# Performance work log

Measured on AMD Instinct MI355X. Metric: run time of the kernel, lower is better.

The kernel has to match this reference:

```python
import jax, jax.numpy as jnp
import numpy as np

MARGIN = 0.5
BETA = 0.0
K = 5

def setup_inputs() -> dict:
    key = jax.random.key(0)
    k1, k2 = jax.random.split(key)
    n, d, n_classes = 4096, 512, 512
    inputs = jax.random.normal(k1, (n, d), dtype=jnp.float32)
    # L2-normalize as is standard for similarity-based DML embeddings
    inputs = inputs / jnp.linalg.norm(inputs, axis=1, keepdims=True)
    targets = jax.random.randint(k2, (n,), 0, n_classes, dtype=jnp.int64)
    return {"inputs": inputs, "targets": targets}

def reference(inputs, targets):
    n = inputs.shape[0]
    sim = inputs @ inputs.T                      # [n, n] similarity matrix
    same = targets[:, None] == targets[None, :]  # [n, n] same-class mask
    eye = jnp.eye(n, dtype=bool)
    pos_mask = same & ~eye                       # positive pairs (off-diagonal)
    neg_mask = ~same                             # negative pairs
    # margin_loss (hinge on similarity): pos -> [margin + beta - s]_+, neg -> [margin + s - beta]_+
    pos_l = jnp.maximum(MARGIN + BETA - sim, 0.0)
    neg_l = jnp.maximum(MARGIN + sim - BETA, 0.0)
    valid = pos_mask | neg_mask
    pair_loss = jnp.where(pos_mask, pos_l, neg_l)  # per-pair loss where valid
    num_of_zeros = jnp.sum(valid & (pair_loss == 0.0))
    # top-(4K) over the multiset of all valid pair losses (== topk of concat(pos_loss, neg_loss))
    masked = jnp.where(valid, pair_loss, -jnp.inf).reshape(-1)
    top_loss, _ = jax.lax.top_k(masked, 4 * K)
    loss = jnp.mean(top_loss)
    mean_pos_sim = jnp.sum(jnp.where(pos_mask, sim, 0.0)) / jnp.sum(pos_mask)
    mean_neg_sim = jnp.sum(jnp.where(neg_mask, sim, 0.0)) / jnp.sum(neg_mask)
    # NOTE: the original swaps the names: it returns mean(pos_sim) as `mean_neg_sim` and vice versa.
    return (loss, num_of_zeros, mean_pos_sim, mean_neg_sim)
```

## Files before the change

### kernel.cpp

```cpp
#include <hip/hip_runtime.h>
#include <hip/hip_fp16.h>

constexpr int N = 4096;
constexpr int D = 512;
constexpr int NT = 64;
constexpr int NBLK = NT * (NT + 1) / 2;
constexpr int NSEG = 32;
constexpr int SEGSZ = NBLK / NSEG;
constexpr float SENT = -1e30f;

typedef _Float16 f16x8 __attribute__((ext_vector_type(8)));
typedef float f32x4 __attribute__((ext_vector_type(4)));

__device__ __forceinline__ void load_lds16(const _Float16* g, _Float16* l) {
  __builtin_amdgcn_global_load_lds(
      (const __attribute__((address_space(1))) void*)g,
      (__attribute__((address_space(3))) void*)l, 16, 0, 0);
}

template <int M>
__device__ __forceinline__ void wave_sel10(float (&vals)[M], float (&out)[10]) {
  int lane = threadIdx.x & 63;
  float lm = vals[0];
#pragma unroll
  for (int k = 1; k < M; k++) lm = fmaxf(lm, vals[k]);
#pragma unroll
  for (int r = 0; r < 10; r++) {
    float wmx = lm;
#pragma unroll
    for (int ofs = 1; ofs < 64; ofs <<= 1)
      wmx = fmaxf(wmx, __shfl_xor(wmx, ofs));
    out[r] = wmx;
    unsigned long long b = __ballot(lm == wmx);
    int leader = __ffsll(b) - 1;
    if (lane == leader) {
      bool found = false;
#pragma unroll
      for (int k = 0; k < M; k++) {
        bool hit = !found && (vals[k] == wmx);
        vals[k] = hit ? SENT : vals[k];
        found = found || hit;
      }
      lm = vals[0];
#pragma unroll
      for (int k = 1; k < M; k++) lm = fmaxf(lm, vals[k]);
    }
  }
}

constexpr int TOP10G_OFF = 41600;
constexpr int STATSL2_OFF = 124800;
constexpr int T10L2_OFF = 125440;
constexpr int DONE2_OFF = 126720;
constexpr int XH_OFF = 126976;

__global__ void prep_kernel(const float4* __restrict__ X4,
                            ushort4* __restrict__ Xh4,
                            unsigned* __restrict__ done2) {
  int gid = blockIdx.x * 256 + threadIdx.x;
  if (gid == 0) *done2 = 0u;
  float4 v = X4[gid];
  ushort4 o;
  o.x = __half_as_ushort(__float2half_rn(v.x));
  o.y = __half_as_ushort(__float2half_rn(v.y));
  o.z = __half_as_ushort(__float2half_rn(v.z));
  o.w = __half_as_ushort(__float2half_rn(v.w));
  Xh4[gid] = o;
}

__global__ __launch_bounds__(256, 4) void gemm_stats_kernel(
    const _Float16* __restrict__ Xh, const int* __restrict__ tgt,
    float* __restrict__ slots, float* __restrict__ top10g) {
  float* blk_sumv = slots;
  float* blk_sump = slots + NBLK;
  unsigned* blk_cntv = (unsigned*)(slots + 2 * NBLK);
  unsigned* blk_cntp = (unsigned*)(slots + 3 * NBLK);
  unsigned* blk_zero = (unsigned*)(slots + 4 * NBLK);

  __shared__ _Float16 As[64 * 64];
  __shared__ _Float16 Bs[64 * 64];
  __shared__ int tA[64], tB[64];
  __shared__ float redf[2][4];
  __shared__ unsigned redu[3][4];
  __shared__ float wml[40];

  int tid = threadIdx.x;

  int id = blockIdx.x, br = 0;
  while (id >= (NT - br)) { id -= (NT - br); br++; }
  int bc = br + id;

  if (tid < 64) tA[tid] = tgt[br * 64 + tid];
  else if (tid < 128) tB[tid - 64] = tgt[bc * 64 + (tid - 64)];

  int lane = tid & 63, wave = tid >> 6;
  int wm = (wave >> 1) << 5;
  int wn = (wave & 1) << 5;
  int lrow = lane & 15;
  int q4 = lane >> 4;
  int x7 = lrow & 7;
  int quad4 = q4 * 4;

  int srow[2], scol[2], sdst[2];
#pragma unroll
  for (int i = 0; i < 2; i++) {
    int C = (i * 4 + wave) * 64 + lane;
    int row = C >> 3, p = C & 7;
    srow[i] = row;
    scol[i] = (p ^ (row & 7)) * 8;
    sdst[i] = (i * 4 + wave) * 512;
  }
  const _Float16* Arow = Xh + (size_t)(br * 64) * D;
  const _Float16* Brow = Xh + (size_t)(bc * 64) * D;

  f32x4 acc[2][2] = {};

  for (int k0 = 0; k0 < D; k0 += 64) {
    __syncthreads();
#pragma unroll
    for (int i = 0; i < 2; i++) {
      load_lds16(Arow + srow[i] * D + k0 + scol[i], As + sdst[i]);
      load_lds16(Brow + srow[i] * D + k0 + scol[i], Bs + sdst[i]);
    }
    __syncthreads();
#pragma unroll
    for (int ks = 0; ks < 64; ks += 32) {
      int c0 = ks >> 3;
      f16x8 af[2], bf[2];
#pragma unroll
      for (int mi = 0; mi < 2; mi++)
        af[mi] = *(const f16x8*)&As[(wm + mi * 16 + lrow) * 64 +
                                    ((c0 + q4) ^ x7) * 8];
#pragma unroll
      for (int ni = 0; ni < 2; ni++)
        bf[ni] = *(const f16x8*)&Bs[(wn + ni * 16 + lrow) * 64 +
                                    ((c0 + q4) ^ x7) * 8];
#pragma unroll
      for (int mi = 0; mi < 2; mi++)
#pragma unroll
        for (int ni = 0; ni < 2; ni++)
          acc[mi][ni] = __builtin_amdgcn_mfma_f32_16x16x32_f16(
              af[mi], bf[ni], acc[mi][ni], 0, 0, 0);
    }
  }

  int ti2[2][4], tj2[2];
#pragma unroll
  for (int ni = 0; ni < 2; ni++) tj2[ni] = tB[wn + ni * 16 + lrow];
#pragma unroll
  for (int mi = 0; mi < 2; mi++)
#pragma unroll
    for (int r = 0; r < 4; r++) ti2[mi][r] = tA[wm + mi * 16 + quad4 + r];

  float lsv = 0.f, lsp = 0.f;
  unsigned lcv = 0, lcp = 0, lz = 0;
  int ibase = br * 64 + wm + quad4;
  int jbase = bc * 64 + wn + lrow;

  float vals[16];
#pragma unroll
  for (int mi = 0; mi < 2; mi++)
#pragma unroll
    for (int ni = 0; ni < 2; ni++)
#pragma unroll
      for (int r = 0; r < 4; r++) {
        float s = acc[mi][ni][r];
        int i = ibase + mi * 16 + r;
        int j = jbase + ni * 16;
        bool valid = j > i;
        bool pos = valid && (ti2[mi][r] == tj2[ni]);
        float t = pos ? -s : s;
        float loss = fmaxf(0.5f + t, 0.0f);
        if (valid) { lsv += s; lcv++; if (loss == 0.0f) lz++; }
        if (pos) { lsp += s; lcp++; }
        vals[(mi * 2 + ni) * 4 + r] = valid ? loss : SENT;
      }

#pragma unroll
  for (int o = 32; o > 0; o >>= 1) {
    lsv += __shfl_down(lsv, o);
    lsp += __shfl_down(lsp, o);
    lcv += __shfl_down(lcv, o);
    lcp += __shfl_down(lcp, o);
    lz  += __shfl_down(lz, o);
  }
  if (lane == 0) {
    redf[0][wave] = lsv; redf[1][wave] = lsp;
    redu[0][wave] = lcv; redu[1][wave] = lcp; redu[2][wave] = lz;
  }

  float wl[10];
  wave_sel10<16>(vals, wl);
  if (lane == 0) {
#pragma unroll
    for (int r = 0; r < 10; r++) wml[wave * 10 + r] = wl[r];
  }
  __syncthreads();

  if (wave == 0) {
    float mv[1];
    mv[0] = (lane < 40) ? wml[lane] : SENT;
    float b10[10];
    wave_sel10<1>(mv, b10);
    if (lane == 0) {
      int b = blockIdx.x;
      blk_sumv[b] = redf[0][0] + redf[0][1] + redf[0][2] + redf[0][3];
      blk_sump[b] = redf[1][0] + redf[1][1] + redf[1][2] + redf[1][3];
      blk_cntv[b] = redu[0][0] + redu[0][1] + redu[0][2] + redu[0][3];
      blk_cntp[b] = redu[1][0] + redu[1][1] + redu[1][2] + redu[1][3];
      blk_zero[b] = redu[2][0] + redu[2][1] + redu[2][2] + redu[2][3];
#pragma unroll
      for (int r = 0; r < 10; r++) top10g[b * 10 + r] = b10[r];
    }
  }
}

__global__ __launch_bounds__(256) void finalize_kernel(
    const float* __restrict__ slots, const float* __restrict__ top10g,
    float* __restrict__ statsL2, float* __restrict__ t10L2,
    unsigned* __restrict__ done2, float* __restrict__ out) {
  const float* blk_sumv = slots;
  const float* blk_sump = slots + NBLK;
  const unsigned* blk_cntv = (const unsigned*)(slots + 2 * NBLK);
  const unsigned* blk_cntp = (const unsigned*)(slots + 3 * NBLK);
  const unsigned* blk_zero = (const unsigned*)(slots + 4 * NBLK);

  __shared__ float wml[40];
  __shared__ float redf[2][4];
  __shared__ unsigned redu[3][4];
  __shared__ int lastFlag;

  int tid = threadIdx.x;
  int lane = tid & 63, wave = tid >> 6;
  int f = blockIdx.x;

  float sv = 0.f, sp = 0.f;
  unsigned cv = 0, cp = 0, zz = 0;
  if (tid < SEGSZ) {
    int row = f * SEGSZ + tid;
    sv = blk_sumv[row]; sp = blk_sump[row];
    cv = blk_cntv[row]; cp = blk_cntp[row]; zz = blk_zero[row];
  }
#pragma unroll
  for (int o = 32; o > 0; o >>= 1) {
    sv += __shfl_down(sv, o);
    sp += __shfl_down(sp, o);
    cv += __shfl_down(cv, o);
    cp += __shfl_down(cp, o);
    zz += __shfl_down(zz, o);
  }
  if (lane == 0) {
    redf[0][wave] = sv; redf[1][wave] = sp;
    redu[0][wave] = cv; redu[1][wave] = cp; redu[2][wave] = zz;
  }

  float v3[3];
#pragma unroll
  for (int k = 0; k < 3; k++) {
    int g = tid + k * 256;
    v3[k] = (g < SEGSZ * 10) ? top10g[f * SEGSZ * 10 + g] : SENT;
  }
  float wl[10];
  wave_sel10<3>(v3, wl);
  if (lane == 0) {
#pragma unroll
    for (int r = 0; r < 10; r++) wml[wave * 10 + r] = wl[r];
  }
  __syncthreads();
  if (wave == 0) {
    float mv[1];
    mv[0] = (lane < 40) ? wml[lane] : SENT;
    float s10[10];
    wave_sel10<1>(mv, s10);
    if (lane == 0) {
      statsL2[f] = redf[0][0] + redf[0][1] + redf[0][2] + redf[0][3];
      statsL2[NSEG + f] = redf[1][0] + redf[1][1] + redf[1][2] + redf[1][3];
      ((unsigned*)statsL2)[2 * NSEG + f] =
          redu[0][0] + redu[0][1] + redu[0][2] + redu[0][3];
      ((unsigned*)statsL2)[3 * NSEG + f] =
          redu[1][0] + redu[1][1] + redu[1][2] + redu[1][3];
      ((unsigned*)statsL2)[4 * NSEG + f] =
          redu[2][0] + redu[2][1] + redu[2][2] + redu[2][3];
#pragma unroll
      for (int r = 0; r < 10; r++) t10L2[f * 10 + r] = s10[r];
    }
  }
  __syncthreads();

  if (tid == 0) {
    __threadfence();
    unsigned old = atomicAdd(done2, 1u);
    lastFlag = (old == NSEG - 1);
  }
  __syncthreads();
  if (!lastFlag) return;
  __threadfence();

  float sv2 = 0.f, sp2 = 0.f;
  unsigned cv2 = 0, cp2 = 0, zz2 = 0;
  if (tid < NSEG) {
    sv2 = statsL2[tid]; sp2 = statsL2[NSEG + tid];
    cv2 = ((const unsigned*)statsL2)[2 * NSEG + tid];
    cp2 = ((const unsigned*)statsL2)[3 * NSEG + tid];
    zz2 = ((const unsigned*)statsL2)[4 * NSEG + tid];
  }
#pragma unroll
  for (int o = 32; o > 0; o >>= 1) {
    sv2 += __shfl_down(sv2, o);
    sp2 += __shfl_down(sp2, o);
    cv2 += __shfl_down(cv2, o);
    cp2 += __shfl_down(cp2, o);
    zz2 += __shfl_down(zz2, o);
  }
  if (lane == 0) {
    redf[0][wave] = sv2; redf[1][wave] = sp2;
    redu[0][wave] = cv2; redu[1][wave] = cp2; redu[2][wave] = zz2;
  }

  float v2[2];
  v2[0] = (tid < NSEG * 10) ? t10L2[tid] : SENT;
  int g2 = tid + 256;
  v2[1] = (g2 < NSEG * 10) ? t10L2[g2] : SENT;
  float wl2[10];
  wave_sel10<2>(v2, wl2);
  if (lane == 0) {
#pragma unroll
    for (int r = 0; r < 10; r++) wml[wave * 10 + r] = wl2[r];
  }
  __syncthreads();

  if (wave == 0) {
    float mv[1];
    mv[0] = (lane < 40) ? wml[lane] : SENT;
    float f10[10];
    wave_sel10<1>(mv, f10);
    if (lane == 0) {
      float topsum = 0.f;
#pragma unroll
      for (int r = 0; r < 10; r++) topsum += f10[r];
      float tsv = redf[0][0] + redf[0][1] + redf[0][2] + redf[0][3];
      float tsp = redf[1][0] + redf[1][1] + redf[1][2] + redf[1][3];
      unsigned tcv = redu[0][0] + redu[0][1] + redu[0][2] + redu[0][3];
      unsigned tcp = redu[1][0] + redu[1][1] + redu[1][2] + redu[1][3];
      unsigned tzz = redu[2][0] + redu[2][1] + redu[2][2] + redu[2][3];
      out[0] = topsum * 0.1f;
      out[1] = (float)(2u * tzz);
      out[2] = tsp / (float)tcp;
      out[3] = (tsv - tsp) / (float)(tcv - tcp);
    }
  }
}

extern "C" void kernel_launch(void* const* d_in, const int* in_sizes, int n_in,
                              void* d_out, int out_size, void* d_ws, size_t ws_size,
                              hipStream_t stream) {
  const float* X = (const float*)d_in[0];
  const int* tgt = (const int*)d_in[1];
  float* out = (float*)d_out;
  char* ws = (char*)d_ws;

  float* slots = (float*)ws;
  float* top10g = (float*)(ws + TOP10G_OFF);
  float* statsL2 = (float*)(ws + STATSL2_OFF);
  float* t10L2 = (float*)(ws + T10L2_OFF);
  unsigned* done2 = (unsigned*)(ws + DONE2_OFF);
  _Float16* Xh = (_Float16*)(ws + XH_OFF);

  prep_kernel<<<(N * D / 4) / 256, 256, 0, stream>>>((const float4*)X,
                                                     (ushort4*)Xh, done2);
  gemm_stats_kernel<<<NBLK, 256, 0, stream>>>(Xh, tgt, slots, top10g);
  finalize_kernel<<<NSEG, 256, 0, stream>>>(slots, top10g, statsL2, t10L2,
                                            done2, out);
}
```

Before: 107.1 us.

## Use 128x128 double-buffered tiles, per-wave max, and recompute candidate tiles for top-k

Moves from 64x64 to 128x128 triangular tiles with 512 threads and double-buffered LDS loads. Each block no longer does a per-wave top-10 selection; it keeps only a per-wave maximum loss. A single finalize block takes the 10th-largest of those maxima as a threshold, recomputes the GEMM only for sub-tiles whose max reaches it, and collects the losses above it for the final top-10. The valid-pair count is hardcoded, and positive and zero counts are packed into 16-bit halves of one counter. The candidate and value buffers are capped and could overflow, and the recompute runs serially in one block.

```diff
diff --git a/kernel.cpp b/kernel.cpp
--- a/kernel.cpp
+++ b/kernel.cpp
@@ -3,11 +3,11 @@
 
 constexpr int N = 4096;
 constexpr int D = 512;
-constexpr int NT = 64;
+constexpr int NT = 32;
 constexpr int NBLK = NT * (NT + 1) / 2;
-constexpr int NSEG = 32;
-constexpr int SEGSZ = NBLK / NSEG;
+constexpr int NWM = NBLK * 8;
 constexpr float SENT = -1e30f;
+constexpr unsigned TCV = 8386560u;
 
 typedef _Float16 f16x8 __attribute__((ext_vector_type(8)));
 typedef float f32x4 __attribute__((ext_vector_type(4)));
@@ -48,17 +48,11 @@
   }
 }
 
-constexpr int TOP10G_OFF = 41600;
-constexpr int STATSL2_OFF = 124800;
-constexpr int T10L2_OFF = 125440;
-constexpr int DONE2_OFF = 126720;
-constexpr int XH_OFF = 126976;
+constexpr int XH_OFF = 32768;
 
 __global__ void prep_kernel(const float4* __restrict__ X4,
-                            ushort4* __restrict__ Xh4,
-                            unsigned* __restrict__ done2) {
+                            ushort4* __restrict__ Xh4) {
   int gid = blockIdx.x * 256 + threadIdx.x;
-  if (gid == 0) *done2 = 0u;
   float4 v = X4[gid];
   ushort4 o;
   o.x = __half_as_ushort(__float2half_rn(v.x));
@@ -68,21 +62,14 @@
   Xh4[gid] = o;
 }
 
-__global__ __launch_bounds__(256, 4) void gemm_stats_kernel(
+__global__ __launch_bounds__(512, 4) void gemm_stats_kernel(
     const _Float16* __restrict__ Xh, const int* __restrict__ tgt,
-    float* __restrict__ slots, float* __restrict__ top10g) {
-  float* blk_sumv = slots;
-  float* blk_sump = slots + NBLK;
-  unsigned* blk_cntv = (unsigned*)(slots + 2 * NBLK);
-  unsigned* blk_cntp = (unsigned*)(slots + 3 * NBLK);
-  unsigned* blk_zero = (unsigned*)(slots + 4 * NBLK);
-
-  __shared__ _Float16 As[64 * 64];
-  __shared__ _Float16 Bs[64 * 64];
-  __shared__ int tA[64], tB[64];
-  __shared__ float redf[2][4];
-  __shared__ unsigned redu[3][4];
-  __shared__ float wml[40];
+    float* __restrict__ slots) {
+  __shared__ _Float16 As[2][128 * 64];
+  __shared__ _Float16 Bs[2][128 * 64];
+  __shared__ int tA[128], tB[128];
+  __shared__ float redf[2][8];
+  __shared__ unsigned redu[8];
 
   int tid = threadIdx.x;
 
@@ -90,12 +77,12 @@
   while (id >= (NT - br)) { id -= (NT - br); br++; }
   int bc = br + id;
 
-  if (tid < 64) tA[tid] = tgt[br * 64 + tid];
-  else if (tid < 128) tB[tid - 64] = tgt[bc * 64 + (tid - 64)];
+  if (tid < 128) tA[tid] = tgt[br * 128 + tid];
+  else if (tid < 256) tB[tid - 128] = tgt[bc * 128 + (tid - 128)];
 
   int lane = tid & 63, wave = tid >> 6;
-  int wm = (wave >> 1) << 5;
-  int wn = (wave & 1) << 5;
+  int wm2 = (wave >> 2) << 6;
+  int wn2 = (wave & 3) << 5;
   int lrow = lane & 15;
   int q4 = lane >> 4;
   int x7 = lrow & 7;
@@ -104,39 +91,48 @@
   int srow[2], scol[2], sdst[2];
 #pragma unroll
   for (int i = 0; i < 2; i++) {
-    int C = (i * 4 + wave) * 64 + lane;
+    int C = i * 512 + tid;
     int row = C >> 3, p = C & 7;
     srow[i] = row;
     scol[i] = (p ^ (row & 7)) * 8;
-    sdst[i] = (i * 4 + wave) * 512;
-  }
-  const _Float16* Arow = Xh + (size_t)(br * 64) * D;
-  const _Float16* Brow = Xh + (size_t)(bc * 64) * D;
-
-  f32x4 acc[2][2] = {};
-
-  for (int k0 = 0; k0 < D; k0 += 64) {
+    sdst[i] = (i * 8 + wave) * 512;
+  }
+  const _Float16* Arow = Xh + (size_t)(br * 128) * D;
+  const _Float16* Brow = Xh + (size_t)(bc * 128) * D;
+
+#pragma unroll
+  for (int i = 0; i < 2; i++) {
+    load_lds16(Arow + srow[i] * D + scol[i], &As[0][sdst[i]]);
+    load_lds16(Brow + srow[i] * D + scol[i], &Bs[0][sdst[i]]);
+  }
+
+  f32x4 acc[4][2] = {};
+#pragma unroll
+  for (int t = 0; t < 8; t++) {
+    int cur = t & 1;
     __syncthreads();
-#pragma unroll
-    for (int i = 0; i < 2; i++) {
-      load_lds16(Arow + srow[i] * D + k0 + scol[i], As + sdst[i]);
-      load_lds16(Brow + srow[i] * D + k0 + scol[i], Bs + sdst[i]);
-    }
-    __syncthreads();
+    if (t < 7) {
+      int k0 = (t + 1) * 64;
+#pragma unroll
+      for (int i = 0; i < 2; i++) {
+        load_lds16(Arow + srow[i] * D + k0 + scol[i], &As[cur ^ 1][sdst[i]]);
+        load_lds16(Brow + srow[i] * D + k0 + scol[i], &Bs[cur ^ 1][sdst[i]]);
+      }
+    }
 #pragma unroll
     for (int ks = 0; ks < 64; ks += 32) {
       int c0 = ks >> 3;
-      f16x8 af[2], bf[2];
-#pragma unroll
-      for (int mi = 0; mi < 2; mi++)
-        af[mi] = *(const f16x8*)&As[(wm + mi * 16 + lrow) * 64 +
-                                    ((c0 + q4) ^ x7) * 8];
+      f16x8 af[4], bf[2];
+#pragma unroll
+      for (int mi = 0; mi < 4; mi++)
+        af[mi] = *(const f16x8*)&As[cur][(wm2 + mi * 16 + lrow) * 64 +
+                                         ((c0 + q4) ^ x7) * 8];
 #pragma unroll
       for (int ni = 0; ni < 2; ni++)
-        bf[ni] = *(const f16x8*)&Bs[(wn + ni * 16 + lrow) * 64 +
-                                    ((c0 + q4) ^ x7) * 8];
-#pragma unroll
-      for (int mi = 0; mi < 2; mi++)
+        bf[ni] = *(const f16x8*)&Bs[cur][(wn2 + ni * 16 + lrow) * 64 +
+                                         ((c0 + q4) ^ x7) * 8];
+#pragma unroll
+      for (int mi = 0; mi < 4; mi++)
 #pragma unroll
         for (int ni = 0; ni < 2; ni++)
           acc[mi][ni] = __builtin_amdgcn_mfma_f32_16x16x32_f16(
@@ -144,231 +140,258 @@
     }
   }
 
-  int ti2[2][4], tj2[2];
-#pragma unroll
-  for (int ni = 0; ni < 2; ni++) tj2[ni] = tB[wn + ni * 16 + lrow];
-#pragma unroll
-  for (int mi = 0; mi < 2; mi++)
-#pragma unroll
-    for (int r = 0; r < 4; r++) ti2[mi][r] = tA[wm + mi * 16 + quad4 + r];
-
-  float lsv = 0.f, lsp = 0.f;
-  unsigned lcv = 0, lcp = 0, lz = 0;
-  int ibase = br * 64 + wm + quad4;
-  int jbase = bc * 64 + wn + lrow;
-
-  float vals[16];
-#pragma unroll
-  for (int mi = 0; mi < 2; mi++)
-#pragma unroll
-    for (int ni = 0; ni < 2; ni++)
-#pragma unroll
-      for (int r = 0; r < 4; r++) {
+  int tj[2];
+#pragma unroll
+  for (int ni = 0; ni < 2; ni++) tj[ni] = tB[wn2 + ni * 16 + lrow];
+
+  float lsv = 0.f, lsp = 0.f, lmax = SENT;
+  unsigned cz = 0;
+  int ib = br * 128 + wm2 + quad4;
+  int jb = bc * 128 + wn2 + lrow;
+#pragma unroll
+  for (int mi = 0; mi < 4; mi++) {
+#pragma unroll
+    for (int r = 0; r < 4; r++) {
+      int trow = tA[wm2 + mi * 16 + quad4 + r];
+      int i = ib + mi * 16 + r;
+#pragma unroll
+      for (int ni = 0; ni < 2; ni++) {
         float s = acc[mi][ni][r];
-        int i = ibase + mi * 16 + r;
-        int j = jbase + ni * 16;
+        int j = jb + ni * 16;
         bool valid = j > i;
-        bool pos = valid && (ti2[mi][r] == tj2[ni]);
-        float t = pos ? -s : s;
-        float loss = fmaxf(0.5f + t, 0.0f);
-        if (valid) { lsv += s; lcv++; if (loss == 0.0f) lz++; }
-        if (pos) { lsp += s; lcp++; }
-        vals[(mi * 2 + ni) * 4 + r] = valid ? loss : SENT;
+        bool pos = valid && (trow == tj[ni]);
+        float loss = fmaxf(0.5f + (pos ? -s : s), 0.0f);
+        if (valid) { lsv += s; if (loss == 0.0f) cz += 0x10000u; }
+        if (pos) { lsp += s; cz += 1u; }
+        lmax = fmaxf(lmax, valid ? loss : SENT);
       }
-
+    }
+  }
 #pragma unroll
   for (int o = 32; o > 0; o >>= 1) {
     lsv += __shfl_down(lsv, o);
     lsp += __shfl_down(lsp, o);
-    lcv += __shfl_down(lcv, o);
-    lcp += __shfl_down(lcp, o);
-    lz  += __shfl_down(lz, o);
+    cz += __shfl_down(cz, o);
+    lmax = fmaxf(lmax, __shfl_down(lmax, o));
   }
   if (lane == 0) {
-    redf[0][wave] = lsv; redf[1][wave] = lsp;
-    redu[0][wave] = lcv; redu[1][wave] = lcp; redu[2][wave] = lz;
-  }
-
-  float wl[10];
-  wave_sel10<16>(vals, wl);
-  if (lane == 0) {
-#pragma unroll
-    for (int r = 0; r < 10; r++) wml[wave * 10 + r] = wl[r];
-  }
-  __syncthreads();
-
-  if (wave == 0) {
-    float mv[1];
-    mv[0] = (lane < 40) ? wml[lane] : SENT;
-    float b10[10];
-    wave_sel10<1>(mv, b10);
-    if (lane == 0) {
-      int b = blockIdx.x;
-      blk_sumv[b] = redf[0][0] + redf[0][1] + redf[0][2] + redf[0][3];
-      blk_sump[b] = redf[1][0] + redf[1][1] + redf[1][2] + redf[1][3];
-      blk_cntv[b] = redu[0][0] + redu[0][1] + redu[0][2] + redu[0][3];
-      blk_cntp[b] = redu[1][0] + redu[1][1] + redu[1][2] + redu[1][3];
-      blk_zero[b] = redu[2][0] + redu[2][1] + redu[2][2] + redu[2][3];
-#pragma unroll
-      for (int r = 0; r < 10; r++) top10g[b * 10 + r] = b10[r];
-    }
-  }
-}
-
-__global__ __launch_bounds__(256) void finalize_kernel(
-    const float* __restrict__ slots, const float* __restrict__ top10g,
-    float* __restrict__ statsL2, float* __restrict__ t10L2,
-    unsigned* __restrict__ done2, float* __restrict__ out) {
-  const float* blk_sumv = slots;
-  const float* blk_sump = slots + NBLK;
-  const unsigned* blk_cntv = (const unsigned*)(slots + 2 * NBLK);
-  const unsigned* blk_cntp = (const unsigned*)(slots + 3 * NBLK);
-  const unsigned* blk_zero = (const unsigned*)(slots + 4 * NBLK);
-
-  __shared__ float wml[40];
-  __shared__ float redf[2][4];
-  __shared__ unsigned redu[3][4];
-  __shared__ int lastFlag;
-
-  int tid = threadIdx.x;
-  int lane = tid & 63, wave = tid >> 6;
-  int f = blockIdx.x;
+    redf[0][wave] = lsv; redf[1][wave] = lsp; redu[wave] = cz;
+    slots[3 * NBLK + blockIdx.x * 8 + wave] = lmax;
+  }
+  __syncthreads();
+  if (tid == 0) {
+    float a = 0.f, b = 0.f;
+    unsigned c = 0;
+#pragma unroll
+    for (int w = 0; w < 8; w++) { a += redf[0][w]; b += redf[1][w]; c += redu[w]; }
+    slots[blockIdx.x] = a;
+    slots[NBLK + blockIdx.x] = b;
+    ((unsigned*)slots)[2 * NBLK + blockIdx.x] = c;
+  }
+}
+
+__device__ __forceinline__ void load_frags(const _Float16* __restrict__ Xh,
+                                           int r0, int c0, int kk, int lrow,
+                                           int q4, f16x8 (&af)[4],
+                                           f16x8 (&bf)[2]) {
+#pragma unroll
+  for (int mi = 0; mi < 4; mi++)
+    af[mi] = *(const f16x8*)&Xh[(size_t)(r0 + mi * 16 + lrow) * D + kk + q4 * 8];
+#pragma unroll
+  for (int ni = 0; ni < 2; ni++)
+    bf[ni] = *(const f16x8*)&Xh[(size_t)(c0 + ni * 16 + lrow) * D + kk + q4 * 8];
+}
+
+__device__ __forceinline__ void mfma8(f32x4 (&a4)[4][2], f16x8 (&af)[4],
+                                      f16x8 (&bf)[2]) {
+#pragma unroll
+  for (int mi = 0; mi < 4; mi++)
+#pragma unroll
+    for (int ni = 0; ni < 2; ni++)
+      a4[mi][ni] = __builtin_amdgcn_mfma_f32_16x16x32_f16(af[mi], bf[ni],
+                                                          a4[mi][ni], 0, 0, 0);
+}
+
+__global__ __launch_bounds__(512) void finalize_kernel(
+    const _Float16* __restrict__ Xh, const int* __restrict__ tgt,
+    const float* __restrict__ slots, float* __restrict__ out) {
+  const float* sumv = slots;
+  const float* sump = slots + NBLK;
+  const unsigned* cnts = (const unsigned*)(slots + 2 * NBLK);
+  const float* wmax = slots + 3 * NBLK;
+
+  __shared__ float svals[2048];
+  __shared__ int scand[1024];
+  __shared__ float wml[80];
+  __shared__ float redf[2][8];
+  __shared__ unsigned redu2[2][8];
+  __shared__ float sres[2];
+  __shared__ unsigned scnt2[2];
+  __shared__ unsigned snc, snv;
+  __shared__ float sT;
+
+  int tid = threadIdx.x, lane = tid & 63, wave = tid >> 6;
+  if (tid == 0) { snc = 0u; snv = 0u; }
 
   float sv = 0.f, sp = 0.f;
-  unsigned cv = 0, cp = 0, zz = 0;
-  if (tid < SEGSZ) {
-    int row = f * SEGSZ + tid;
-    sv = blk_sumv[row]; sp = blk_sump[row];
-    cv = blk_cntv[row]; cp = blk_cntp[row]; zz = blk_zero[row];
+  unsigned cp = 0, zz = 0;
+#pragma unroll
+  for (int k = 0; k < 2; k++) {
+    int r = tid + k * 512;
+    if (r < NBLK) {
+      sv += sumv[r]; sp += sump[r];
+      unsigned c = cnts[r];
+      cp += c & 0xffffu; zz += c >> 16;
+    }
+  }
+  float mv[9], keep[9];
+#pragma unroll
+  for (int k = 0; k < 9; k++) {
+    int g = tid + k * 512;
+    mv[k] = (g < NWM) ? wmax[g] : SENT;
+    keep[k] = mv[k];
   }
 #pragma unroll
   for (int o = 32; o > 0; o >>= 1) {
-    sv += __shfl_down(sv, o);
-    sp += __shfl_down(sp, o);
-    cv += __shfl_down(cv, o);
-    cp += __shfl_down(cp, o);
-    zz += __shfl_down(zz, o);
+    sv += __shfl_down(sv, o); sp += __shfl_down(sp, o);
+    cp += __shfl_down(cp, o); zz += __shfl_down(zz, o);
   }
   if (lane == 0) {
     redf[0][wave] = sv; redf[1][wave] = sp;
-    redu[0][wave] = cv; redu[1][wave] = cp; redu[2][wave] = zz;
-  }
-
-  float v3[3];
-#pragma unroll
-  for (int k = 0; k < 3; k++) {
-    int g = tid + k * 256;
-    v3[k] = (g < SEGSZ * 10) ? top10g[f * SEGSZ * 10 + g] : SENT;
+    redu2[0][wave] = cp; redu2[1][wave] = zz;
   }
   float wl[10];
-  wave_sel10<3>(v3, wl);
+  wave_sel10<9>(mv, wl);
   if (lane == 0) {
 #pragma unroll
     for (int r = 0; r < 10; r++) wml[wave * 10 + r] = wl[r];
   }
   __syncthreads();
+  if (tid == 0) {
+    float a = 0.f, b = 0.f;
+    unsigned c = 0, z = 0;
+#pragma unroll
+    for (int w = 0; w < 8; w++) {
+      a += redf[0][w]; b += redf[1][w];
+      c += redu2[0][w]; z += redu2[1][w];
+    }
+    sres[0] = a; sres[1] = b; scnt2[0] = c; scnt2[1] = z;
+  }
   if (wave == 0) {
-    float mv[1];
-    mv[0] = (lane < 40) ? wml[lane] : SENT;
-    float s10[10];
-    wave_sel10<1>(mv, s10);
-    if (lane == 0) {
-      statsL2[f] = redf[0][0] + redf[0][1] + redf[0][2] + redf[0][3];
-      statsL2[NSEG + f] = redf[1][0] + redf[1][1] + redf[1][2] + redf[1][3];
-      ((unsigned*)statsL2)[2 * NSEG + f] =
-          redu[0][0] + redu[0][1] + redu[0][2] + redu[0][3];
-      ((unsigned*)statsL2)[3 * NSEG + f] =
-          redu[1][0] + redu[1][1] + redu[1][2] + redu[1][3];
-      ((unsigned*)statsL2)[4 * NSEG + f] =
-          redu[2][0] + redu[2][1] + redu[2][2] + redu[2][3];
-#pragma unroll
-      for (int r = 0; r < 10; r++) t10L2[f * 10 + r] = s10[r];
-    }
-  }
-  __syncthreads();
-
-  if (tid == 0) {
-    __threadfence();
-    unsigned old = atomicAdd(done2, 1u);
-    lastFlag = (old == NSEG - 1);
-  }
-  __syncthreads();
-  if (!lastFlag) return;
-  __threadfence();
-
-  float sv2 = 0.f, sp2 = 0.f;
-  unsigned cv2 = 0, cp2 = 0, zz2 = 0;
-  if (tid < NSEG) {
-    sv2 = statsL2[tid]; sp2 = statsL2[NSEG + tid];
-    cv2 = ((const unsigned*)statsL2)[2 * NSEG + tid];
-    cp2 = ((const unsigned*)statsL2)[3 * NSEG + tid];
-    zz2 = ((const unsigned*)statsL2)[4 * NSEG + tid];
-  }
-#pragma unroll
-  for (int o = 32; o > 0; o >>= 1) {
-    sv2 += __shfl_down(sv2, o);
-    sp2 += __shfl_down(sp2, o);
-    cv2 += __shfl_down(cv2, o);
-    cp2 += __shfl_down(cp2, o);
-    zz2 += __shfl_down(zz2, o);
-  }
+    float m2[2];
+    m2[0] = wml[lane];
+    m2[1] = (lane + 64 < 80) ? wml[lane + 64] : SENT;
+    float t10[10];
+    wave_sel10<2>(m2, t10);
+    if (lane == 0) sT = t10[9];
+  }
+  __syncthreads();
+  float T = sT;
+
+#pragma unroll
+  for (int k = 0; k < 9; k++) {
+    int g = tid + k * 512;
+    if (g < NWM && keep[k] >= T) {
+      unsigned p = atomicAdd(&snc, 1u);
+      if (p < 1024u) scand[p] = g;
+    }
+  }
+  __syncthreads();
+
+  int nu = (int)snc;
+  if (nu > 1024) nu = 1024;
+  int lrow = lane & 15, q4 = lane >> 4, quad4 = q4 * 4;
+  for (int u = wave; u < nu; u += 8) {
+    int g = scand[u];
+    int cb = g >> 3, wr = g & 7;
+    int idd = cb, br = 0;
+    while (idd >= (NT - br)) { idd -= (NT - br); br++; }
+    int bc = br + idd;
+    int r0 = br * 128 + ((wr >> 2) << 6);
+    int c0 = bc * 128 + ((wr & 3) << 5);
+
+    f32x4 a4[4][2] = {};
+    f16x8 af0[4], bf0[2], af1[4], bf1[2];
+    load_frags(Xh, r0, c0, 0, lrow, q4, af0, bf0);
+#pragma unroll
+    for (int kk = 0; kk < D; kk += 64) {
+      load_frags(Xh, r0, c0, kk + 32, lrow, q4, af1, bf1);
+      mfma8(a4, af0, bf0);
+      if (kk + 64 < D) load_frags(Xh, r0, c0, kk + 64, lrow, q4, af0, bf0);
+      mfma8(a4, af1, bf1);
+    }
+    int tj[2];
+#pragma unroll
+    for (int ni = 0; ni < 2; ni++) tj[ni] = tgt[c0 + ni * 16 + lrow];
+#pragma unroll
+    for (int mi = 0; mi < 4; mi++) {
+#pragma unroll
+      for (int r = 0; r < 4; r++) {
+        int i = r0 + mi * 16 + quad4 + r;
+        int trow = tgt[i];
+#pragma unroll
+        for (int ni = 0; ni < 2; ni++) {
+          int j = c0 + ni * 16 + lrow;
+          float s = a4[mi][ni][r];
+          bool valid = j > i;
+          bool pos = valid && (trow == tj[ni]);
+          float loss = fmaxf(0.5f + (pos ? -s : s), 0.0f);
+          if (valid && loss >= T) {
+            unsigned p = atomicAdd(&snv, 1u);
+            if (p < 2048u) svals[p] = loss;
+          }
+        }
+      }
+    }
+  }
+  __syncthreads();
+
+  int nv = (int)snv;
+  if (nv > 2048) nv = 2048;
+  float v4[4];
+#pragma unroll
+  for (int k = 0; k < 4; k++) {
+    int g = tid + k * 512;
+    v4[k] = (g < nv) ? svals[g] : SENT;
+  }
+  float wl2[10];
+  wave_sel10<4>(v4, wl2);
   if (lane == 0) {
-    redf[0][wave] = sv2; redf[1][wave] = sp2;
-    redu[0][wave] = cv2; redu[1][wave] = cp2; redu[2][wave] = zz2;
-  }
-
-  float v2[2];
-  v2[0] = (tid < NSEG * 10) ? t10L2[tid] : SENT;
-  int g2 = tid + 256;
-  v2[1] = (g2 < NSEG * 10) ? t10L2[g2] : SENT;
-  float wl2[10];
-  wave_sel10<2>(v2, wl2);
-  if (lane == 0) {
 #pragma unroll
     for (int r = 0; r < 10; r++) wml[wave * 10 + r] = wl2[r];
   }
   __syncthreads();
-
   if (wave == 0) {
-    float mv[1];
-    mv[0] = (lane < 40) ? wml[lane] : SENT;
+    float m2[2];
+    m2[0] = wml[lane];
+    m2[1] = (lane + 64 < 80) ? wml[lane + 64] : SENT;
     float f10[10];
-    wave_sel10<1>(mv, f10);
+    wave_sel10<2>(m2, f10);
     if (lane == 0) {
       float topsum = 0.f;
 #pragma unroll
       for (int r = 0; r < 10; r++) topsum += f10[r];
-      float tsv = redf[0][0] + redf[0][1] + redf[0][2] + redf[0][3];
-      float tsp = redf[1][0] + redf[1][1] + redf[1][2] + redf[1][3];
-      unsigned tcv = redu[0][0] + redu[0][1] + redu[0][2] + redu[0][3];
-      unsigned tcp = redu[1][0] + redu[1][1] + redu[1][2] + redu[1][3];
-      unsigned tzz = redu[2][0] + redu[2][1] + redu[2][2] + redu[2][3];
       out[0] = topsum * 0.1f;
-      out[1] = (float)(2u * tzz);
-      out[2] = tsp / (float)tcp;
-      out[3] = (tsv - tsp) / (float)(tcv - tcp);
+      out[1] = (float)(2u * scnt2[1]);
+      out[2] = sres[1] / (float)scnt2[0];
+      out[3] = (sres[0] - sres[1]) / (float)(TCV - scnt2[0]);
     }
   }
 }
 
 extern "C" void kernel_launch(void* const* d_in, const int* in_sizes, int n_in,
-                              void* d_out, int out_size, void* d_ws, size_t ws_size,
-                              hipStream_t stream) {
+                              void* d_out, int out_size, void* d_ws,
+                              size_t ws_size, hipStream_t stream) {
   const float* X = (const float*)d_in[0];
   const int* tgt = (const int*)d_in[1];
   float* out = (float*)d_out;
   char* ws = (char*)d_ws;
 
   float* slots = (float*)ws;
-  float* top10g = (float*)(ws + TOP10G_OFF);
-  float* statsL2 = (float*)(ws + STATSL2_OFF);
-  float* t10L2 = (float*)(ws + T10L2_OFF);
-  unsigned* done2 = (unsigned*)(ws + DONE2_OFF);
   _Float16* Xh = (_Float16*)(ws + XH_OFF);
 
   prep_kernel<<<(N * D / 4) / 256, 256, 0, stream>>>((const float4*)X,
-                                                     (ushort4*)Xh, done2);
-  gemm_stats_kernel<<<NBLK, 256, 0, stream>>>(Xh, tgt, slots, top10g);
-  finalize_kernel<<<NSEG, 256, 0, stream>>>(slots, top10g, statsL2, t10L2,
-                                            done2, out);
-}
+                                                     (ushort4*)Xh);
+  gemm_stats_kernel<<<NBLK, 512, 0, stream>>>(Xh, tgt, slots);
+  finalize_kernel<<<1, 512, 0, stream>>>(Xh, tgt, slots, out);
+}
```

After: 126.5 us. 18.0% more time.
